# Kernel tuning notes

Hardware: AMD Instinct MI355X
Metric: run time of the kernel (lower is better)

## Reference

```python
import jax, jax.numpy as jnp
import numpy as np

N_NODES = 50000
N_EDGES = 800000
D_IN = 96
D_EDGE = 32
D_OUT = 96
N_TYPES = 4


def setup_inputs() -> dict:
    key = jax.random.key(0)
    k = jax.random.split(key, 6)
    x = jax.random.normal(k[0], (N_NODES, D_IN), dtype=jnp.float32)
    edge_features = jax.random.normal(k[1], (N_NODES, D_EDGE), dtype=jnp.float32)
    edge_index = jax.random.randint(k[2], (2, N_EDGES), 0, N_NODES, dtype=jnp.int32)
    edge_type = jax.random.randint(k[3], (N_EDGES,), 0, N_TYPES, dtype=jnp.int32)
    # One RelEdgeConv per relation type: Linear(D_IN + D_EDGE -> D_OUT) message fn
    scale = 1.0 / np.sqrt(D_IN + D_EDGE)
    W_msg = jax.random.uniform(k[4], (N_TYPES, D_IN + D_EDGE, D_OUT), jnp.float32, -scale, scale)
    b_msg = jax.random.uniform(k[5], (N_TYPES, D_OUT), jnp.float32, -scale, scale)
    return {"x": x, "edge_features": edge_features, "edge_index": edge_index,
            "edge_type": edge_type, "W_msg": W_msg, "b_msg": b_msg}


def reference(x, edge_features, edge_index, edge_type, W_msg, b_msg):
    # Node-level edge_features (shape[0] == N) -> per-edge relative features
    src, dst = edge_index[0], edge_index[1]
    e = jnp.abs(edge_features[src] - edge_features[dst])          # [E, De]
    feat = jnp.concatenate([x[src], e], axis=-1)                  # [E, Din+De]
    n_nodes = x.shape[0]
    n_types = W_msg.shape[0]

    def per_type(t):
        # relation mask: zero out messages for edges of other types
        mask = (edge_type == t).astype(x.dtype)[:, None]          # [E, 1]
        m = (feat @ W_msg[t] + b_msg[t]) * mask                   # [E, Dout]
        # scatter-add messages to destination nodes
        return jax.ops.segment_sum(m, dst, num_segments=n_nodes)  # [N, Dout]

    out = jnp.stack([per_type(t) for t in range(n_types)])        # [T, N, Dout]
    return out.mean(axis=0)
```

## Files before the change

kernel.cpp:

```cpp
#include <hip/hip_runtime.h>

#define E_EDGES 800000
#define NN 50000
#define D_IN 96
#define D_EDGE 32
#define D_OUT 96
#define KSUM 512
#define SSTRIDE 520
#define NBUCK 196
#define BCAP 4800
#define NCHUNK 256
#define CHE 3125
#define CHIT 13
#define BUILD_BLOCKS 512
#define SUBCAP 768

typedef __attribute__((ext_vector_type(8))) __bf16 bf16x8;
typedef __attribute__((ext_vector_type(4))) float floatx4;

__device__ __forceinline__ float lo16(unsigned int u) {
    return __builtin_bit_cast(float, u << 16);
}
__device__ __forceinline__ float hi16(unsigned int u) {
    return __builtin_bit_cast(float, u & 0xFFFF0000u);
}
__device__ __forceinline__ unsigned int pk2(float a, float b) {
    unsigned short ua = __builtin_bit_cast(unsigned short, (__bf16)a);
    unsigned short ub = __builtin_bit_cast(unsigned short, (__bf16)b);
    return (unsigned int)ua | ((unsigned int)ub << 16);
}

__global__ __launch_bounds__(256) void k_prep(const int* __restrict__ ei,
                                              const int* __restrict__ et,
                                              const float* __restrict__ x,
                                              const float* __restrict__ ef,
                                              const float* __restrict__ Wm,
                                              int* __restrict__ cursor,
                                              int* __restrict__ eb,
                                              __bf16* __restrict__ WT,
                                              unsigned int* __restrict__ xeb) {
    __shared__ int lcnt[NBUCK];
    __shared__ int gbase[NBUCK];
    int tid = threadIdx.x, bid = blockIdx.x;

    if (bid < NCHUNK) {
        int e0 = bid * CHE;
        for (int i = tid; i < NBUCK; i += 256) lcnt[i] = 0;
        __syncthreads();

        int pv[CHIT], br[CHIT];
#pragma unroll
        for (int it = 0; it < CHIT; it++) {
            int i = it * 256 + tid;
            br[it] = -1;
            if (i < CHE) {
                int e = e0 + i;
                int dst = ei[E_EDGES + e];
                int b = dst >> 8;
                int rank = atomicAdd(&lcnt[b], 1);
                pv[it] = ei[e] | (et[e] << 16) | ((dst & 255) << 18);
                br[it] = rank | (b << 16);
            }
        }
        __syncthreads();
        for (int b = tid; b < NBUCK; b += 256)
            gbase[b] = lcnt[b] ? atomicAdd(&cursor[b], lcnt[b]) : 0;
        __syncthreads();
#pragma unroll
        for (int it = 0; it < CHIT; it++) {
            if (br[it] >= 0) {
                int b = br[it] >> 16, rank = br[it] & 0xFFFF;
                int pos = gbase[b] + rank;
                if (pos < BCAP) eb[b * BCAP + pos] = pv[it];
            }
        }
    } else {
        int b2 = bid - NCHUNK;
        int gtid = b2 * 256 + tid;
        int lane = tid & 63, w = tid >> 6;
        for (int n = b2 * 4 + w; n < NN; n += BUILD_BLOCKS * 4) {
            float2 v;
            if (lane < 48) v = *(const float2*)(x  + (size_t)n * D_IN   + 2 * lane);
            else           v = *(const float2*)(ef + (size_t)n * D_EDGE + 2 * (lane - 48));
            xeb[(size_t)n * 64 + lane] = pk2(v.x, v.y);
        }
        for (int i = gtid; i < 96 * KSUM; i += BUILD_BLOCKS * 256) {
            int n = i >> 9, k = i & 511;
            WT[n * KSUM + k] = (__bf16)Wm[(size_t)k * 96 + n];
        }
    }
}

__global__ __launch_bounds__(512) void k_fused(const int* __restrict__ cursor,
                                               const int* __restrict__ eb,
                                               const unsigned int* __restrict__ xeb,
                                               const __bf16* __restrict__ WT,
                                               const float* __restrict__ bm,
                                               float* __restrict__ out) {
    __shared__ __align__(16) __bf16 Sl[32][SSTRIDE];
    __shared__ int elist[SUBCAP];
    __shared__ int cnt32[32], base32[32];
    __shared__ float cnts[32][4];
    __shared__ int tcnt;
    int* ta = (int*)&Sl[0][0];
    int* tb = ta + SUBCAP;

    int tid = threadIdx.x, lane = tid & 63, w = tid >> 6;
    int B = blockIdx.x >> 3, sg = blockIdx.x & 7;
    int seg = B * BCAP;
    int m = min(cursor[B], BCAP);

    if (tid < 32) cnt32[tid] = 0;
    if (tid == 0) tcnt = 0;
    __syncthreads();

    for (int i = tid; i < m; i += 512) {
        int p = eb[seg + i];
        int dl = (p >> 18) & 255;
        if ((dl >> 5) == sg) {
            int nl = dl & 31;
            int slot = atomicAdd(&tcnt, 1);
            int rank = atomicAdd(&cnt32[nl], 1);
            if (slot < SUBCAP) { ta[slot] = p; tb[slot] = (nl << 16) | rank; }
        }
    }
    __syncthreads();

    if (w == 0 && lane < 32) {
        int v = cnt32[lane];
        int s = v;
        for (int d = 1; d < 32; d <<= 1) {
            int t = __shfl_up(s, d, 64);
            if (lane >= d) s += t;
        }
        base32[lane] = s - v;
    }
    __syncthreads();

    int tmax = min(tcnt, SUBCAP);
    for (int i = tid; i < tmax; i += 512) {
        int p = ta[i], pr = tb[i];
        int pos = base32[pr >> 16] + (pr & 0xFFFF);
        if (pos < SUBCAP) elist[pos] = p;
    }
    __syncthreads();

    unsigned int Mmask = (lane >= 48) ? 0x7FFFFFFFu : 0xFFFFFFFFu;

#define ACC(u, ty) do {                                                        \
        float f0 = lo16(u), f1 = hi16(u);                                      \
        f0 = __builtin_bit_cast(float,                                         \
                 __builtin_bit_cast(unsigned int, f0 - e0) & Mmask);           \
        f1 = __builtin_bit_cast(float,                                         \
                 __builtin_bit_cast(unsigned int, f1 - e1) & Mmask);           \
        if      ((ty) == 0) { s0a += f0; s0b += f1; c0++; }                    \
        else if ((ty) == 1) { s1a += f0; s1b += f1; c1++; }                    \
        else if ((ty) == 2) { s2a += f0; s2b += f1; c2++; }                    \
        else                { s3a += f0; s3b += f1; c3++; }                    \
    } while (0)

    for (int j = 0; j < 4; j++) {
        int nl = w * 4 + j;
        int n = B * 256 + sg * 32 + nl;
        int num = cnt32[nl], bs = base32[nl];
        float s0a = 0, s0b = 0, s1a = 0, s1b = 0,
              s2a = 0, s2b = 0, s3a = 0, s3b = 0;
        int c0 = 0, c1 = 0, c2 = 0, c3 = 0;
        float e0 = 0.f, e1 = 0.f;
        if (lane >= 48 && num > 0) {
            unsigned int u = xeb[(size_t)n * 64 + lane];
            e0 = lo16(u); e1 = hi16(u);
        }

        int i = 0;
        for (; i + 7 < num; i += 8) {
            int v0 = elist[bs + i],     v1 = elist[bs + i + 1];
            int v2 = elist[bs + i + 2], v3 = elist[bs + i + 3];
            int v4 = elist[bs + i + 4], v5 = elist[bs + i + 5];
            int v6 = elist[bs + i + 6], v7 = elist[bs + i + 7];
            unsigned int u0 = xeb[(size_t)(v0 & 0xFFFF) * 64 + lane];
            unsigned int u1 = xeb[(size_t)(v1 & 0xFFFF) * 64 + lane];
            unsigned int u2 = xeb[(size_t)(v2 & 0xFFFF) * 64 + lane];
            unsigned int u3 = xeb[(size_t)(v3 & 0xFFFF) * 64 + lane];
            unsigned int u4 = xeb[(size_t)(v4 & 0xFFFF) * 64 + lane];
            unsigned int u5 = xeb[(size_t)(v5 & 0xFFFF) * 64 + lane];
            unsigned int u6 = xeb[(size_t)(v6 & 0xFFFF) * 64 + lane];
            unsigned int u7 = xeb[(size_t)(v7 & 0xFFFF) * 64 + lane];
            ACC(u0, (v0 >> 16) & 3); ACC(u1, (v1 >> 16) & 3);
            ACC(u2, (v2 >> 16) & 3); ACC(u3, (v3 >> 16) & 3);
            ACC(u4, (v4 >> 16) & 3); ACC(u5, (v5 >> 16) & 3);
            ACC(u6, (v6 >> 16) & 3); ACC(u7, (v7 >> 16) & 3);
        }
        for (; i < num; i++) {
            int v = elist[bs + i];
            unsigned int u = xeb[(size_t)(v & 0xFFFF) * 64 + lane];
            ACC(u, (v >> 16) & 3);
        }

        unsigned int* sp = (unsigned int*)&Sl[nl][0];
        sp[  0 + lane] = pk2(s0a, s0b);
        sp[ 64 + lane] = pk2(s1a, s1b);
        sp[128 + lane] = pk2(s2a, s2b);
        sp[192 + lane] = pk2(s3a, s3b);
        if (lane == 0) {
            cnts[nl][0] = (float)c0; cnts[nl][1] = (float)c1;
            cnts[nl][2] = (float)c2; cnts[nl][3] = (float)c3;
        }
    }
#undef ACC
    __syncthreads();

    int quad = lane >> 4, low = lane & 15;
    int rt = w & 1;

    bf16x8 a[16];
    const __bf16* ap = &Sl[rt * 16 + low][0] + quad * 8;
#pragma unroll
    for (int ks = 0; ks < 16; ks++) a[ks] = *(const bf16x8*)(ap + ks * 32);

    for (int t = w; t < 12; t += 8) {
        int ct = t >> 1;
        floatx4 acc = {0.f, 0.f, 0.f, 0.f};
        const __bf16* bp = WT + (size_t)(ct * 16 + low) * KSUM + quad * 8;
#pragma unroll
        for (int ks = 0; ks < 16; ks++)
            acc = __builtin_amdgcn_mfma_f32_16x16x32_bf16(
                a[ks], *(const bf16x8*)(bp + ks * 32), acc, 0, 0, 0);
        int col = ct * 16 + low;
#pragma unroll
        for (int rg = 0; rg < 4; rg++) {
            int r = rt * 16 + quad * 4 + rg;
            int g = B * 256 + sg * 32 + r;
            if (g < NN) {
                float bias = cnts[r][0] * bm[col]       + cnts[r][1] * bm[96 + col]
                           + cnts[r][2] * bm[192 + col] + cnts[r][3] * bm[288 + col];
                out[(size_t)g * D_OUT + col] = 0.25f * (acc[rg] + bias);
            }
        }
    }
}

extern "C" void kernel_launch(void* const* d_in, const int* in_sizes, int n_in,
                              void* d_out, int out_size, void* d_ws, size_t ws_size,
                              hipStream_t stream) {
    const float* x  = (const float*)d_in[0];
    const float* ef = (const float*)d_in[1];
    const int*   ei = (const int*)d_in[2];
    const int*   et = (const int*)d_in[3];
    const float* Wm = (const float*)d_in[4];
    const float* bm = (const float*)d_in[5];
    float* out = (float*)d_out;

    int* cursor = (int*)d_ws;
    int* eb     = cursor + 256;
    __bf16* WT  = (__bf16*)(eb + NBUCK * BCAP);
    unsigned int* xeb = (unsigned int*)(WT + 96 * KSUM);

    hipMemsetAsync(cursor, 0, NBUCK * sizeof(int), stream);
    k_prep <<<NCHUNK + BUILD_BLOCKS, 256, 0, stream>>>(ei, et, x, ef, Wm,
                                                       cursor, eb, WT, xeb);
    k_fused<<<NBUCK * 8, 512, 0, stream>>>(cursor, eb, xeb, WT, bm, out);
}
```

Before: 209.9 us.

## Stage bucket writes locally, split fused blocks to 16 nodes, pre-scale gather offsets

The prep kernel now prefix-sums bucket counts and stages each chunk's edges in shared memory before writing them to global memory, so stores to each bucket are contiguous. The fused kernel uses 256-thread blocks covering 16 destination nodes instead of 512 threads covering 32. It also replaces the atomic-based temporary list with a count-then-scatter pass over the bucket, and derives per-type bias counts from a 64-entry histogram. Packed edge entries now hold the source index already multiplied by 64, removing the per-gather multiply, and the edge type is read with readfirstlane so the branch is wave-uniform. The trade-off is that each bucket is now read twice and by twice as many blocks, and the prep kernel uses more shared memory.

```diff
diff --git a/kernel.cpp b/kernel.cpp
--- a/kernel.cpp
+++ b/kernel.cpp
@@ -13,7 +13,7 @@
 #define CHE 3125
 #define CHIT 13
 #define BUILD_BLOCKS 512
-#define SUBCAP 768
+#define SUBCAP 384
 
 typedef __attribute__((ext_vector_type(8))) __bf16 bf16x8;
 typedef __attribute__((ext_vector_type(4))) float floatx4;
@@ -40,7 +40,11 @@
                                               __bf16* __restrict__ WT,
                                               unsigned int* __restrict__ xeb) {
     __shared__ int lcnt[NBUCK];
-    __shared__ int gbase[NBUCK];
+    __shared__ int lexcl[NBUCK];
+    __shared__ int gb[NBUCK];
+    __shared__ int tmp[256];
+    __shared__ int stage[CHE];
+    __shared__ int spos[CHE];
     int tid = threadIdx.x, bid = blockIdx.x;
 
     if (bid < NCHUNK) {
@@ -58,21 +62,36 @@
                 int dst = ei[E_EDGES + e];
                 int b = dst >> 8;
                 int rank = atomicAdd(&lcnt[b], 1);
-                pv[it] = ei[e] | (et[e] << 16) | ((dst & 255) << 18);
+                pv[it] = (ei[e] << 6) | (et[e] << 22) | ((dst & 255) << 24);
                 br[it] = rank | (b << 16);
             }
         }
         __syncthreads();
+        int v = (tid < NBUCK) ? lcnt[tid] : 0;
+        tmp[tid] = v; __syncthreads();
+        for (int d = 1; d < 256; d <<= 1) {
+            int t = (tid >= d) ? tmp[tid - d] : 0;
+            __syncthreads();
+            tmp[tid] += t; __syncthreads();
+        }
+        if (tid < NBUCK) lexcl[tid] = tmp[tid] - v;
         for (int b = tid; b < NBUCK; b += 256)
-            gbase[b] = lcnt[b] ? atomicAdd(&cursor[b], lcnt[b]) : 0;
+            gb[b] = lcnt[b] ? atomicAdd(&cursor[b], lcnt[b]) : 0;
         __syncthreads();
 #pragma unroll
         for (int it = 0; it < CHIT; it++) {
             if (br[it] >= 0) {
                 int b = br[it] >> 16, rank = br[it] & 0xFFFF;
-                int pos = gbase[b] + rank;
-                if (pos < BCAP) eb[b * BCAP + pos] = pv[it];
+                int lidx = lexcl[b] + rank;
+                stage[lidx] = pv[it];
+                int gp = gb[b] + rank;
+                spos[lidx] = (gp < BCAP) ? (b * BCAP + gp) : -1;
             }
+        }
+        __syncthreads();
+        for (int i = tid; i < CHE; i += 256) {
+            int p = spos[i];
+            if (p >= 0) eb[p] = stage[i];
         }
     } else {
         int b2 = bid - NCHUNK;
@@ -91,81 +110,78 @@
     }
 }
 
-__global__ __launch_bounds__(512) void k_fused(const int* __restrict__ cursor,
+__global__ __launch_bounds__(256) void k_fused(const int* __restrict__ cursor,
                                                const int* __restrict__ eb,
                                                const unsigned int* __restrict__ xeb,
                                                const __bf16* __restrict__ WT,
                                                const float* __restrict__ bm,
                                                float* __restrict__ out) {
-    __shared__ __align__(16) __bf16 Sl[32][SSTRIDE];
+    __shared__ __align__(16) __bf16 Sl[16][SSTRIDE];
     __shared__ int elist[SUBCAP];
-    __shared__ int cnt32[32], base32[32];
-    __shared__ float cnts[32][4];
-    __shared__ int tcnt;
-    int* ta = (int*)&Sl[0][0];
-    int* tb = ta + SUBCAP;
+    __shared__ int cnt64[64];
+    __shared__ int base16[16], c2[16], tot16[16];
 
     int tid = threadIdx.x, lane = tid & 63, w = tid >> 6;
-    int B = blockIdx.x >> 3, sg = blockIdx.x & 7;
+    int B = blockIdx.x >> 4, sg = blockIdx.x & 15;
     int seg = B * BCAP;
     int m = min(cursor[B], BCAP);
 
-    if (tid < 32) cnt32[tid] = 0;
-    if (tid == 0) tcnt = 0;
-    __syncthreads();
-
-    for (int i = tid; i < m; i += 512) {
+    if (tid < 64) cnt64[tid] = 0;
+    __syncthreads();
+
+    for (int i = tid; i < m; i += 256) {
         int p = eb[seg + i];
-        int dl = (p >> 18) & 255;
-        if ((dl >> 5) == sg) {
-            int nl = dl & 31;
-            int slot = atomicAdd(&tcnt, 1);
-            int rank = atomicAdd(&cnt32[nl], 1);
-            if (slot < SUBCAP) { ta[slot] = p; tb[slot] = (nl << 16) | rank; }
-        }
-    }
-    __syncthreads();
-
-    if (w == 0 && lane < 32) {
-        int v = cnt32[lane];
-        int s = v;
-        for (int d = 1; d < 32; d <<= 1) {
+        unsigned int dl = ((unsigned int)p) >> 24;
+        if ((int)(dl >> 4) == sg)
+            atomicAdd(&cnt64[((dl & 15) << 2) | ((p >> 22) & 3)], 1);
+    }
+    __syncthreads();
+
+    if (w == 0 && lane < 16) {
+        int tot = cnt64[lane * 4] + cnt64[lane * 4 + 1]
+                + cnt64[lane * 4 + 2] + cnt64[lane * 4 + 3];
+        tot16[lane] = tot;
+        int s = tot;
+        for (int d = 1; d < 16; d <<= 1) {
             int t = __shfl_up(s, d, 64);
             if (lane >= d) s += t;
         }
-        base32[lane] = s - v;
-    }
-    __syncthreads();
-
-    int tmax = min(tcnt, SUBCAP);
-    for (int i = tid; i < tmax; i += 512) {
-        int p = ta[i], pr = tb[i];
-        int pos = base32[pr >> 16] + (pr & 0xFFFF);
-        if (pos < SUBCAP) elist[pos] = p;
+        base16[lane] = s - tot;
+        c2[lane] = s - tot;
+    }
+    __syncthreads();
+
+    for (int i = tid; i < m; i += 256) {
+        int p = eb[seg + i];
+        unsigned int dl = ((unsigned int)p) >> 24;
+        if ((int)(dl >> 4) == sg) {
+            int pos = atomicAdd(&c2[dl & 15], 1);
+            if (pos < SUBCAP) elist[pos] = p;
+        }
     }
     __syncthreads();
 
     unsigned int Mmask = (lane >= 48) ? 0x7FFFFFFFu : 0xFFFFFFFFu;
 
-#define ACC(u, ty) do {                                                        \
+#define ACCS(u, v) do {                                                        \
         float f0 = lo16(u), f1 = hi16(u);                                      \
         f0 = __builtin_bit_cast(float,                                         \
                  __builtin_bit_cast(unsigned int, f0 - e0) & Mmask);           \
         f1 = __builtin_bit_cast(float,                                         \
                  __builtin_bit_cast(unsigned int, f1 - e1) & Mmask);           \
-        if      ((ty) == 0) { s0a += f0; s0b += f1; c0++; }                    \
-        else if ((ty) == 1) { s1a += f0; s1b += f1; c1++; }                    \
-        else if ((ty) == 2) { s2a += f0; s2b += f1; c2++; }                    \
-        else                { s3a += f0; s3b += f1; c3++; }                    \
+        int sty = (__builtin_amdgcn_readfirstlane(v) >> 22) & 3;               \
+        if      (sty == 0) { s0a += f0; s0b += f1; }                           \
+        else if (sty == 1) { s1a += f0; s1b += f1; }                           \
+        else if (sty == 2) { s2a += f0; s2b += f1; }                           \
+        else               { s3a += f0; s3b += f1; }                           \
     } while (0)
 
     for (int j = 0; j < 4; j++) {
         int nl = w * 4 + j;
-        int n = B * 256 + sg * 32 + nl;
-        int num = cnt32[nl], bs = base32[nl];
+        int n = B * 256 + sg * 16 + nl;
+        int num = tot16[nl], bs = base16[nl];
         float s0a = 0, s0b = 0, s1a = 0, s1b = 0,
               s2a = 0, s2b = 0, s3a = 0, s3b = 0;
-        int c0 = 0, c1 = 0, c2 = 0, c3 = 0;
         float e0 = 0.f, e1 = 0.f;
         if (lane >= 48 && num > 0) {
             unsigned int u = xeb[(size_t)n * 64 + lane];
@@ -178,23 +194,21 @@
             int v2 = elist[bs + i + 2], v3 = elist[bs + i + 3];
             int v4 = elist[bs + i + 4], v5 = elist[bs + i + 5];
             int v6 = elist[bs + i + 6], v7 = elist[bs + i + 7];
-            unsigned int u0 = xeb[(size_t)(v0 & 0xFFFF) * 64 + lane];
-            unsigned int u1 = xeb[(size_t)(v1 & 0xFFFF) * 64 + lane];
-            unsigned int u2 = xeb[(size_t)(v2 & 0xFFFF) * 64 + lane];
-            unsigned int u3 = xeb[(size_t)(v3 & 0xFFFF) * 64 + lane];
-            unsigned int u4 = xeb[(size_t)(v4 & 0xFFFF) * 64 + lane];
-            unsigned int u5 = xeb[(size_t)(v5 & 0xFFFF) * 64 + lane];
-            unsigned int u6 = xeb[(size_t)(v6 & 0xFFFF) * 64 + lane];
-            unsigned int u7 = xeb[(size_t)(v7 & 0xFFFF) * 64 + lane];
-            ACC(u0, (v0 >> 16) & 3); ACC(u1, (v1 >> 16) & 3);
-            ACC(u2, (v2 >> 16) & 3); ACC(u3, (v3 >> 16) & 3);
-            ACC(u4, (v4 >> 16) & 3); ACC(u5, (v5 >> 16) & 3);
-            ACC(u6, (v6 >> 16) & 3); ACC(u7, (v7 >> 16) & 3);
+            unsigned int u0 = xeb[(v0 & 0x3FFFFF) + lane];
+            unsigned int u1 = xeb[(v1 & 0x3FFFFF) + lane];
+            unsigned int u2 = xeb[(v2 & 0x3FFFFF) + lane];
+            unsigned int u3 = xeb[(v3 & 0x3FFFFF) + lane];
+            unsigned int u4 = xeb[(v4 & 0x3FFFFF) + lane];
+            unsigned int u5 = xeb[(v5 & 0x3FFFFF) + lane];
+            unsigned int u6 = xeb[(v6 & 0x3FFFFF) + lane];
+            unsigned int u7 = xeb[(v7 & 0x3FFFFF) + lane];
+            ACCS(u0, v0); ACCS(u1, v1); ACCS(u2, v2); ACCS(u3, v3);
+            ACCS(u4, v4); ACCS(u5, v5); ACCS(u6, v6); ACCS(u7, v7);
         }
         for (; i < num; i++) {
             int v = elist[bs + i];
-            unsigned int u = xeb[(size_t)(v & 0xFFFF) * 64 + lane];
-            ACC(u, (v >> 16) & 3);
+            unsigned int u = xeb[(v & 0x3FFFFF) + lane];
+            ACCS(u, v);
         }
 
         unsigned int* sp = (unsigned int*)&Sl[nl][0];
@@ -202,24 +216,18 @@
         sp[ 64 + lane] = pk2(s1a, s1b);
         sp[128 + lane] = pk2(s2a, s2b);
         sp[192 + lane] = pk2(s3a, s3b);
-        if (lane == 0) {
-            cnts[nl][0] = (float)c0; cnts[nl][1] = (float)c1;
-            cnts[nl][2] = (float)c2; cnts[nl][3] = (float)c3;
-        }
-    }
-#undef ACC
+    }
+#undef ACCS
     __syncthreads();
 
     int quad = lane >> 4, low = lane & 15;
-    int rt = w & 1;
 
     bf16x8 a[16];
-    const __bf16* ap = &Sl[rt * 16 + low][0] + quad * 8;
+    const __bf16* ap = &Sl[low][0] + quad * 8;
 #pragma unroll
     for (int ks = 0; ks < 16; ks++) a[ks] = *(const bf16x8*)(ap + ks * 32);
 
-    for (int t = w; t < 12; t += 8) {
-        int ct = t >> 1;
+    for (int ct = w; ct < 6; ct += 4) {
         floatx4 acc = {0.f, 0.f, 0.f, 0.f};
         const __bf16* bp = WT + (size_t)(ct * 16 + low) * KSUM + quad * 8;
 #pragma unroll
@@ -229,11 +237,13 @@
         int col = ct * 16 + low;
 #pragma unroll
         for (int rg = 0; rg < 4; rg++) {
-            int r = rt * 16 + quad * 4 + rg;
-            int g = B * 256 + sg * 32 + r;
+            int r = quad * 4 + rg;
+            int g = B * 256 + sg * 16 + r;
             if (g < NN) {
-                float bias = cnts[r][0] * bm[col]       + cnts[r][1] * bm[96 + col]
-                           + cnts[r][2] * bm[192 + col] + cnts[r][3] * bm[288 + col];
+                float bias = (float)cnt64[r * 4 + 0] * bm[col]
+                           + (float)cnt64[r * 4 + 1] * bm[96 + col]
+                           + (float)cnt64[r * 4 + 2] * bm[192 + col]
+                           + (float)cnt64[r * 4 + 3] * bm[288 + col];
                 out[(size_t)g * D_OUT + col] = 0.25f * (acc[rg] + bias);
             }
         }
@@ -259,5 +269,5 @@
     hipMemsetAsync(cursor, 0, NBUCK * sizeof(int), stream);
     k_prep <<<NCHUNK + BUILD_BLOCKS, 256, 0, stream>>>(ei, et, x, ef, Wm,
                                                        cursor, eb, WT, xeb);
-    k_fused<<<NBUCK * 8, 512, 0, stream>>>(cursor, eb, xeb, WT, bm, out);
-}
+    k_fused<<<NBUCK * 16, 256, 0, stream>>>(cursor, eb, xeb, WT, bm, out);
+}
```

After: 205.6 us. -2.1%, faster.
